# Optimization experiments

Measured on AMD Instinct MI355X. Metric: run time of the kernel, lower is better.

Reference implementation:

```python
import jax, jax.numpy as jnp
import numpy as np

B, N, C_IN, F, OUT = 32, 1000, 128, 128, 64
RATIOS = (0.8, 0.8)


def setup_inputs() -> dict:
    key = jax.random.key(0)
    ks = jax.random.split(key, 10)
    N_nodes = jax.random.randint(ks[0], (B,), 500, N + 1, dtype=jnp.int32)
    ar = jnp.arange(N)
    mask = (ar[None, :] < N_nodes[:, None]).astype(jnp.float32)  # [B,N]
    A = (jax.random.uniform(ks[1], (B, N, N)) < 0.02).astype(jnp.float32)
    A = A * (1.0 - jnp.eye(N, dtype=jnp.float32))
    A = jnp.maximum(A, A.transpose(0, 2, 1))  # symmetric, no self loops
    A = A * mask[:, :, None] * mask[:, None, :]
    x = jax.random.normal(ks[2], (B, N, C_IN)) * mask[..., None]

    def lin(k, fin, fout):
        bnd = 1.0 / np.sqrt(fin)
        kw, kb = jax.random.split(k)
        W = jax.random.uniform(kw, (fout, fin), minval=-bnd, maxval=bnd)
        b = jax.random.uniform(kb, (fout,), minval=-bnd, maxval=bnd)
        return W, b

    W0, b0 = lin(ks[3], C_IN, F)
    W1, b1 = lin(ks[4], F, F)
    W2, b2 = lin(ks[5], F, F)
    bnd = 1.0 / np.sqrt(F)
    p0 = jax.random.uniform(ks[6], (F, 1), minval=-bnd, maxval=bnd)
    p1 = jax.random.uniform(ks[7], (F, 1), minval=-bnd, maxval=bnd)
    Wfc, bfc = lin(ks[8], F, OUT)
    return dict(x=x, A=A, mask=mask, N_nodes=N_nodes,
                W0=W0, b0=b0, W1=W1, b1=b1, W2=W2, b2=b2,
                p0=p0, p1=p1, Wfc=Wfc, bfc=bfc)


def _gconv(x, A, mask, W, b):
    # K=1 Kipf-Welling conv: L = D^-1/2 (A+I) D^-1/2; relu(Linear(L x)) * mask
    n = A.shape[1]
    A_hat = A + jnp.eye(n, dtype=A.dtype)
    D = (jnp.sum(A_hat, axis=1) + 1e-5) ** -0.5  # [B,N]
    L = D[:, :, None] * A_hat * D[:, None, :]
    h = jnp.einsum('bij,bjc->bic', L, x)
    h = h @ W.T + b
    return jax.nn.relu(h) * mask[..., None]


def _pool(x, A, mask, N_nodes, p, ratio):
    # score each node, drop the N_remove lowest-scoring valid nodes per graph
    y = (x @ p)[..., 0] / jnp.sqrt(jnp.sum(p ** 2))  # [B,N]
    N_remove = (N_nodes.astype(jnp.float32) * (1.0 - ratio)).astype(jnp.int32)
    y_key = jnp.where(mask > 0, y, jnp.inf)  # invalid nodes rank last
    ranks = jnp.argsort(jnp.argsort(y_key, axis=1), axis=1)  # ascending rank
    new_mask = ((ranks >= N_remove[:, None]) & (mask > 0)).astype(x.dtype)
    x = x * jnp.tanh(y)[..., None] * new_mask[..., None]
    A = new_mask[:, :, None] * A * new_mask[:, None, :]
    return x, A, new_mask, N_nodes - N_remove


def reference(x, A, mask, N_nodes, W0, b0, W1, b1, W2, b2, p0, p1, Wfc, bfc):
    h = _gconv(x, A, mask, W0, b0)
    h, A1, m1, n1 = _pool(h, A, mask, N_nodes, p0, RATIOS[0])
    h = _gconv(h, A1, m1, W1, b1)
    h, A2, m2, n2 = _pool(h, A1, m1, n1, p1, RATIOS[1])
    h = _gconv(h, A2, m2, W2, b2)
    g = jnp.max(h, axis=1)  # [B,F] global max pool
    return g @ Wfc.T + bfc  # [B,OUT]
```

## Files before the change

### kernel.cpp

```cpp
#include <hip/hip_runtime.h>
#include <math.h>

#define BB 32
#define NN 1000
#define CC 128
#define FF 128
#define OO 64
#define CAP 128
#define NB 40

#define RMC ((float)(1.0 - 0.8))

__global__ void k_csr(const float* __restrict__ A, const float* __restrict__ mask,
                      const int* __restrict__ Nn,
                      const float* __restrict__ p0, const float* __restrict__ p1,
                      const float* __restrict__ W0, const float* __restrict__ W1,
                      const float* __restrict__ W2,
                      short* __restrict__ idx, int* __restrict__ cnt,
                      float* __restrict__ D, float* __restrict__ dg,
                      float* __restrict__ m, float* __restrict__ gate,
                      int* __restrict__ ncur0, float* __restrict__ pn,
                      float* __restrict__ Wt){
  int i = blockIdx.x, b = blockIdx.y, lane = threadIdx.x;
  if (i == NN){
    for (int j = lane; j < NN; j += 64){
      float v = mask[b*NN + j]; m[b*NN + j] = v; gate[b*NN + j] = v;
    }
    if (lane == 0) ncur0[b] = Nn[b];
    if (b == 0 && lane == 1){ float s=0.f; for(int c=0;c<FF;c++) s += p0[c]*p0[c]; pn[0] = sqrtf(s); }
    if (b == 1 && lane == 1){ float s=0.f; for(int c=0;c<FF;c++) s += p1[c]*p1[c]; pn[1] = sqrtf(s); }
    for (int e = b*1536 + lane; e < (b+1)*1536; e += 64){
      int s = e / (FF*CC), rem = e % (FF*CC);
      int c = rem >> 7, f = rem & 127;
      const float* W = (s == 0) ? W0 : (s == 1) ? W1 : W2;
      Wt[(size_t)s*FF*CC + rem] = W[f*CC + c];
    }
    return;
  }
  if (mask[b*NN + i] == 0.f){
    if (lane == 0){
      cnt[b*NN + i] = 0;
      D[b*NN + i]  = 1.0f / sqrtf(1.0f + 1e-5f);
      dg[b*NN + i] = 0.f;
    }
    return;
  }
  const float4* row = (const float4*)(A + ((size_t)b*NN + i)*NN);
  short* out = idx + ((size_t)b*NN + i)*CAP;
  int count = 0;
  for (int base = 0; base < 250; base += 64){
    int q = base + lane;
    float4 v;
    if (q < 250) v = row[q]; else { v.x=v.y=v.z=v.w=0.f; }
    int lc = (v.x!=0.f) + (v.y!=0.f) + (v.z!=0.f) + (v.w!=0.f);
    int pre = lc;
    #pragma unroll
    for (int off = 1; off < 64; off <<= 1){
      int t = __shfl_up(pre, off);
      if (lane >= off) pre += t;
    }
    int tot = __shfl(pre, 63);
    pre -= lc;
    int slot = count + pre;
    int j = q*4;
    if (v.x!=0.f && slot < CAP) out[slot++] = (short)j;
    if (v.y!=0.f && slot < CAP) out[slot++] = (short)(j+1);
    if (v.z!=0.f && slot < CAP) out[slot++] = (short)(j+2);
    if (v.w!=0.f && slot < CAP) out[slot++] = (short)(j+3);
    count += tot;
  }
  if (lane == 0){
    int cn = (count < CAP) ? count : CAP;
    cnt[b*NN + i] = cn;
    float Dv = 1.0f / sqrtf((float)cn + 1.0f + 1e-5f);
    D[b*NN + i]  = Dv;
    dg[b*NN + i] = Dv;
  }
}

__global__ void k_aggt(const short* __restrict__ idx, const int* __restrict__ cnt,
                       const float* __restrict__ D, const float* __restrict__ dg,
                       const float* __restrict__ m, const float* __restrict__ gate,
                       const float* __restrict__ h, float* __restrict__ T){
  __shared__ int   nb[4][CAP];
  __shared__ float dn[4][CAP];
  int blk = blockIdx.x;
  int b   = (blk & 7) + 8*((blk >> 3) & 3);
  int rem = blk >> 5;
  int tid = threadIdx.x;
  int w = tid >> 6, lane = tid & 63;
  int i = rem*4 + w;
  int g = lane >> 5, l32 = lane & 31;
  size_t orow = ((size_t)b*NN + i)*CC;
  const float* hb = h + (size_t)b*NN*CC;
  if (m[b*NN + i] == 0.f){
    if (g == 0){ float4 z = {0.f,0.f,0.f,0.f}; *(float4*)(T + orow + (l32<<2)) = z; }
    return;
  }
  int n = cnt[b*NN + i];
  const short* r = idx + ((size_t)b*NN + i)*CAP;
  int*   nbw = nb[w];
  float* dnw = dn[w];
  int j0 = 0; float d0 = 0.f; bool k0 = false;
  if (lane < n){ j0 = (int)r[lane]; d0 = dg[b*NN + j0]; k0 = (d0 != 0.f); }
  unsigned long long bal = __ballot(k0);
  int pre = __popcll(bal & ((1ull << lane) - 1ull));
  if (k0){ nbw[pre] = j0*CC; dnw[pre] = d0; }
  int nlive = __popcll(bal);
  if (n > 64){
    int e = lane + 64; int j1 = 0; float d1 = 0.f; bool k1 = false;
    if (e < n){ j1 = (int)r[e]; d1 = dg[b*NN + j1]; k1 = (d1 != 0.f); }
    unsigned long long bal1 = __ballot(k1);
    int pre1 = __popcll(bal1 & ((1ull << lane) - 1ull));
    if (k1){ nbw[nlive + pre1] = j1*CC; dnw[nlive + pre1] = d1; }
    nlive += __popcll(bal1);
  }
  int np = (nlive + 7) & ~7;
  if (lane < np - nlive){ nbw[nlive + lane] = 0; dnw[nlive + lane] = 0.f; }
  __builtin_amdgcn_wave_barrier();
  float4 a0 = {0.f,0.f,0.f,0.f}, a1 = a0, a2 = a0, a3 = a0;
  for (int k = 0; k < np; k += 8){
    int e = k + g;
    float4 v0 = *(const float4*)(hb + nbw[e  ] + (l32<<2));
    float4 v1 = *(const float4*)(hb + nbw[e+2] + (l32<<2));
    float4 v2 = *(const float4*)(hb + nbw[e+4] + (l32<<2));
    float4 v3 = *(const float4*)(hb + nbw[e+6] + (l32<<2));
    float e0 = dnw[e], e1 = dnw[e+2], e2 = dnw[e+4], e3 = dnw[e+6];
    a0.x += e0*v0.x; a0.y += e0*v0.y; a0.z += e0*v0.z; a0.w += e0*v0.w;
    a1.x += e1*v1.x; a1.y += e1*v1.y; a1.z += e1*v1.z; a1.w += e1*v1.w;
    a2.x += e2*v2.x; a2.y += e2*v2.y; a2.z += e2*v2.z; a2.w += e2*v2.w;
    a3.x += e3*v3.x; a3.y += e3*v3.y; a3.z += e3*v3.z; a3.w += e3*v3.w;
  }
  float4 Y;
  Y.x = (a0.x + a1.x) + (a2.x + a3.x);
  Y.y = (a0.y + a1.y) + (a2.y + a3.y);
  Y.z = (a0.z + a1.z) + (a2.z + a3.z);
  Y.w = (a0.w + a1.w) + (a2.w + a3.w);
  Y.x += __shfl_xor(Y.x, 32);
  Y.y += __shfl_xor(Y.y, 32);
  Y.z += __shfl_xor(Y.z, 32);
  Y.w += __shfl_xor(Y.w, 32);
  float Di = D[b*NN + i];
  float gi = gate[b*NN + i];
  if (g == 0){
    float4 hv = *(const float4*)(hb + (size_t)i*CC + (l32<<2));
    float4 o;
    o.x = Di*Y.x + Di*Di*(gi*hv.x);
    o.y = Di*Y.y + Di*Di*(gi*hv.y);
    o.z = Di*Y.z + Di*Di*(gi*hv.z);
    o.w = Di*Y.w + Di*Di*(gi*hv.w);
    *(float4*)(T + orow + (l32<<2)) = o;
  }
}

__global__ void k_lin(const float* __restrict__ T, const float* __restrict__ m,
                      const float* __restrict__ Wt,
                      const float* __restrict__ bias, float* __restrict__ Hout){
  __shared__ float t[NB][CC];
  int b = blockIdx.y, tid = threadIdx.x;
  int i0 = blockIdx.x * NB;
  const float4* Tg = (const float4*)(T + ((size_t)b*NN + i0)*CC);
  float4* tl = (float4*)&t[0][0];
  #pragma unroll
  for (int e = 0; e < 5; e++) tl[tid + e*256] = Tg[tid + e*256];
  __syncthreads();
  int fg = tid & 31;
  int nr = tid >> 5;
  float acc[5][4];
  float4 bi = ((const float4*)bias)[fg];
  #pragma unroll
  for (int n5 = 0; n5 < 5; n5++){
    acc[n5][0]=bi.x; acc[n5][1]=bi.y; acc[n5][2]=bi.z; acc[n5][3]=bi.w;
  }
  for (int c4 = 0; c4 < 32; c4++){
    float4 tv[5];
    #pragma unroll
    for (int n5 = 0; n5 < 5; n5++)
      tv[n5] = *((const float4*)&t[nr + n5*8][c4*4]);
    #pragma unroll
    for (int k = 0; k < 4; k++){
      float4 wv = ((const float4*)Wt)[(size_t)(c4*4 + k)*32 + fg];
      #pragma unroll
      for (int n5 = 0; n5 < 5; n5++){
        float tvv = (k==0) ? tv[n5].x : (k==1) ? tv[n5].y : (k==2) ? tv[n5].z : tv[n5].w;
        acc[n5][0] += tvv*wv.x; acc[n5][1] += tvv*wv.y;
        acc[n5][2] += tvv*wv.z; acc[n5][3] += tvv*wv.w;
      }
    }
  }
  #pragma unroll
  for (int n5 = 0; n5 < 5; n5++){
    int i = i0 + nr + n5*8;
    float mi = m[b*NN + i];
    float4 o4;
    o4.x = fmaxf(acc[n5][0], 0.f)*mi;
    o4.y = fmaxf(acc[n5][1], 0.f)*mi;
    o4.z = fmaxf(acc[n5][2], 0.f)*mi;
    o4.w = fmaxf(acc[n5][3], 0.f)*mi;
    ((float4*)&Hout[((size_t)b*NN + i)*CC])[fg] = o4;
  }
}

__global__ void k_score(const float* __restrict__ H, const float* __restrict__ p,
                        const float* __restrict__ pn, float* __restrict__ y){
  int i = blockIdx.x, b = blockIdx.y, lane = threadIdx.x;
  const float* hrow = H + ((size_t)b*NN + i)*CC;
  float s = hrow[lane]*p[lane] + hrow[lane+64]*p[lane+64];
  for (int off = 32; off > 0; off >>= 1) s += __shfl_down(s, off);
  if (lane == 0) y[b*NN + i] = s / pn[0];
}

__global__ void k_pool(const float* __restrict__ y, float* __restrict__ m,
                       const int* __restrict__ ncur_in, int* __restrict__ ncur_out,
                       float* __restrict__ gate){
  __shared__ float yk[NN];
  int b = blockIdx.y, tid = threadIdx.x;
  int i = blockIdx.x*256 + tid;
  for (int j = tid; j < NN; j += 256)
    yk[j] = (m[b*NN + j] > 0.f) ? y[b*NN + j] : INFINITY;
  __syncthreads();
  int n = ncur_in[b];
  int nr = (int)((float)n * RMC);
  float myv = (i < NN) ? yk[i] : INFINITY;
  int cnt = 0;
  const float4* yk4 = (const float4*)yk;
  #pragma unroll 5
  for (int q = 0; q < 250; q++){
    float4 v = yk4[q];
    int j0 = q*4;
    cnt += (int)((v.x < myv) || (v.x == myv && j0     < i));
    cnt += (int)((v.y < myv) || (v.y == myv && j0 + 1 < i));
    cnt += (int)((v.z < myv) || (v.z == myv && j0 + 2 < i));
    cnt += (int)((v.w < myv) || (v.w == myv && j0 + 3 < i));
  }
  if (i < NN){
    bool keep = (cnt >= nr) && (m[b*NN + i] > 0.f);
    m[b*NN + i]    = keep ? 1.0f : 0.0f;
    gate[b*NN + i] = keep ? tanhf(y[b*NN + i]) : 0.0f;
  }
  if (blockIdx.x == 0 && tid == 0) ncur_out[b] = n - nr;
}

__global__ void k_deg(const short* __restrict__ idx, const int* __restrict__ cnt,
                      const float* __restrict__ m, const float* __restrict__ gate,
                      float* __restrict__ D, float* __restrict__ dg){
  __shared__ float ml[NN];
  int b = blockIdx.y, tid = threadIdx.x;
  for (int i = tid; i < NN; i += 256) ml[i] = m[b*NN + i];
  __syncthreads();
  int j = blockIdx.x*250 + tid;
  if (tid < 250){
    const short* r = idx + ((size_t)b*NN + j)*CAP;
    int n = cnt[b*NN + j];
    float s0=0.f, s1=0.f, s2=0.f, s3=0.f;
    int k = 0;
    for (; k+4 <= n; k += 4){
      s0 += ml[r[k]]; s1 += ml[r[k+1]]; s2 += ml[r[k+2]]; s3 += ml[r[k+3]];
    }
    for (; k < n; k++) s0 += ml[r[k]];
    float Dv = 1.0f / sqrtf(((s0+s1)+(s2+s3)) + 1.0f + 1e-5f);
    D[b*NN + j]  = Dv;
    dg[b*NN + j] = Dv * gate[b*NN + j];
  }
}

__global__ void k_fmax(const float* __restrict__ H, const float* __restrict__ m,
                       float* __restrict__ part){
  int sx = blockIdx.x, b = blockIdx.y, c = threadIdx.x;
  float mx = 0.f;
  int i0 = sx*125;
  for (int i = i0; i < i0+125; i++){
    if (m[b*NN + i] != 0.f)
      mx = fmaxf(mx, H[((size_t)b*NN + i)*CC + c]);
  }
  part[((size_t)b*8 + sx)*CC + c] = mx;
}

__global__ void k_fc(const float* __restrict__ part, const float* __restrict__ Wfc,
                     const float* __restrict__ bfc, float* __restrict__ out){
  __shared__ float g[FF];
  int b = blockIdx.x, tid = threadIdx.x;
  float mx = 0.f;
  #pragma unroll
  for (int s = 0; s < 8; s++) mx = fmaxf(mx, part[((size_t)b*8 + s)*CC + tid]);
  g[tid] = mx;
  __syncthreads();
  if (tid < OO){
    float acc = bfc[tid];
    for (int c = 0; c < FF; c++) acc += g[c]*Wfc[tid*FF + c];
    out[b*OO + tid] = acc;
  }
}

extern "C" void kernel_launch(void* const* d_in, const int* in_sizes, int n_in,
                              void* d_out, int out_size, void* d_ws, size_t ws_size,
                              hipStream_t stream) {
  const float* x    = (const float*)d_in[0];
  const float* A    = (const float*)d_in[1];
  const float* mask = (const float*)d_in[2];
  const int*   Nn   = (const int*)  d_in[3];
  const float* W0   = (const float*)d_in[4];
  const float* b0   = (const float*)d_in[5];
  const float* W1   = (const float*)d_in[6];
  const float* b1   = (const float*)d_in[7];
  const float* W2   = (const float*)d_in[8];
  const float* b2   = (const float*)d_in[9];
  const float* p0   = (const float*)d_in[10];
  const float* p1   = (const float*)d_in[11];
  const float* Wfc  = (const float*)d_in[12];
  const float* bfc  = (const float*)d_in[13];
  float* out = (float*)d_out;

  char* w = (char*)d_ws;
  float* H   = (float*)w; w += (size_t)BB*NN*CC*4;
  float* T   = (float*)w; w += (size_t)BB*NN*CC*4;
  short* idx = (short*)w; w += (size_t)BB*NN*CAP*2;
  float* Wt  = (float*)w; w += (size_t)3*FF*CC*4;
  float* part= (float*)w; w += (size_t)8*BB*CC*4;
  int*   cnt = (int*)w;   w += (size_t)BB*NN*4;
  float* D   = (float*)w; w += (size_t)BB*NN*4;
  float* m   = (float*)w; w += (size_t)BB*NN*4;
  float* ysc = (float*)w; w += (size_t)BB*NN*4;
  float* gate= (float*)w; w += (size_t)BB*NN*4;
  float* dg  = (float*)w; w += (size_t)BB*NN*4;
  int*   ncur= (int*)w;   w += 3*BB*sizeof(int);
  float* pn  = (float*)w; w += 64;

  k_csr<<<dim3(NN + 1, BB), 64, 0, stream>>>(A, mask, Nn, p0, p1, W0, W1, W2,
                                             idx, cnt, D, dg, m, gate, ncur, pn, Wt);

  k_aggt<<<(BB*NN)/4, 256, 0, stream>>>(idx, cnt, D, dg, m, gate, x, T);
  k_lin<<<dim3(25, BB), 256, 0, stream>>>(T, m, Wt + 0*FF*CC, b0, H);
  k_score<<<dim3(NN, BB), 64, 0, stream>>>(H, p0, pn + 0, ysc);
  k_pool<<<dim3(4, BB), 256, 0, stream>>>(ysc, m, ncur + 0*BB, ncur + 1*BB, gate);
  k_deg<<<dim3(4, BB), 256, 0, stream>>>(idx, cnt, m, gate, D, dg);

  k_aggt<<<(BB*NN)/4, 256, 0, stream>>>(idx, cnt, D, dg, m, gate, H, T);
  k_lin<<<dim3(25, BB), 256, 0, stream>>>(T, m, Wt + 1*FF*CC, b1, H);
  k_score<<<dim3(NN, BB), 64, 0, stream>>>(H, p1, pn + 1, ysc);
  k_pool<<<dim3(4, BB), 256, 0, stream>>>(ysc, m, ncur + 1*BB, ncur + 2*BB, gate);
  k_deg<<<dim3(4, BB), 256, 0, stream>>>(idx, cnt, m, gate, D, dg);

  k_aggt<<<(BB*NN)/4, 256, 0, stream>>>(idx, cnt, D, dg, m, gate, H, T);
  k_lin<<<dim3(25, BB), 256, 0, stream>>>(T, m, Wt + 2*FF*CC, b2, H);

  k_fmax<<<dim3(8, BB), 128, 0, stream>>>(H, m, part);
  k_fc<<<BB, 128, 0, stream>>>(part, Wfc, bfc, out);
}
```

Baseline: 465.2 us.

## Fuse score, pool and degree kernels; merge max-pool with final FC

Replaces the separate score, rank-pool and degree kernels with a single per-graph kernel of 1024 threads that computes scores into shared memory, ranks nodes, updates mask and gate, and recomputes degree normalisation. The global max pool and final linear layer are also combined into one kernel. This removes several launches and the global-memory round trips through the intermediate score, mask and partial-max buffers. The cost is that each stage now runs on only 32 blocks (one per graph), which leaves much of the GPU idle and serialises the score computation within a block.

```diff
diff --git a/kernel.cpp b/kernel.cpp
--- a/kernel.cpp
+++ b/kernel.cpp
@@ -201,93 +201,100 @@
   }
 }
 
-__global__ void k_score(const float* __restrict__ H, const float* __restrict__ p,
-                        const float* __restrict__ pn, float* __restrict__ y){
-  int i = blockIdx.x, b = blockIdx.y, lane = threadIdx.x;
-  const float* hrow = H + ((size_t)b*NN + i)*CC;
-  float s = hrow[lane]*p[lane] + hrow[lane+64]*p[lane+64];
-  for (int off = 32; off > 0; off >>= 1) s += __shfl_down(s, off);
-  if (lane == 0) y[b*NN + i] = s / pn[0];
-}
-
-__global__ void k_pool(const float* __restrict__ y, float* __restrict__ m,
-                       const int* __restrict__ ncur_in, int* __restrict__ ncur_out,
-                       float* __restrict__ gate){
+__global__ void k_spd(const float* __restrict__ H, const float* __restrict__ p,
+                      const float* __restrict__ pn,
+                      const short* __restrict__ idx, const int* __restrict__ cnt,
+                      float* __restrict__ m, float* __restrict__ gate,
+                      const int* __restrict__ ncur_in, int* __restrict__ ncur_out,
+                      float* __restrict__ D, float* __restrict__ dg){
   __shared__ float yk[NN];
-  int b = blockIdx.y, tid = threadIdx.x;
-  int i = blockIdx.x*256 + tid;
-  for (int j = tid; j < NN; j += 256)
-    yk[j] = (m[b*NN + j] > 0.f) ? y[b*NN + j] : INFINITY;
+  __shared__ float ml[NN];
+  int b = blockIdx.x, tid = threadIdx.x;
+  int w = tid >> 6, lane = tid & 63;
+  float pl0 = p[lane], pl1 = p[lane + 64];
+  float pnv = pn[0];
+  for (int r = 0; r < 63; r++){
+    int i = w + (r << 4);
+    if (i < NN){
+      const float* hrow = H + ((size_t)b*NN + i)*CC;
+      float s = hrow[lane]*pl0 + hrow[lane+64]*pl1;
+      for (int off = 32; off > 0; off >>= 1) s += __shfl_down(s, off);
+      if (lane == 0) yk[i] = s / pnv;
+    }
+  }
+  __syncthreads();
+  float mold = 0.f;
+  if (tid < NN){
+    mold = m[b*NN + tid];
+    float v = yk[tid];
+    yk[tid] = (mold > 0.f) ? v : INFINITY;
+  }
   __syncthreads();
   int n = ncur_in[b];
   int nr = (int)((float)n * RMC);
+  int i = tid;
   float myv = (i < NN) ? yk[i] : INFINITY;
-  int cnt = 0;
+  int cn = 0;
   const float4* yk4 = (const float4*)yk;
   #pragma unroll 5
   for (int q = 0; q < 250; q++){
     float4 v = yk4[q];
     int j0 = q*4;
-    cnt += (int)((v.x < myv) || (v.x == myv && j0     < i));
-    cnt += (int)((v.y < myv) || (v.y == myv && j0 + 1 < i));
-    cnt += (int)((v.z < myv) || (v.z == myv && j0 + 2 < i));
-    cnt += (int)((v.w < myv) || (v.w == myv && j0 + 3 < i));
-  }
+    cn += (int)((v.x < myv) || (v.x == myv && j0     < i));
+    cn += (int)((v.y < myv) || (v.y == myv && j0 + 1 < i));
+    cn += (int)((v.z < myv) || (v.z == myv && j0 + 2 < i));
+    cn += (int)((v.w < myv) || (v.w == myv && j0 + 3 < i));
+  }
+  float gv = 0.f;
   if (i < NN){
-    bool keep = (cnt >= nr) && (m[b*NN + i] > 0.f);
+    bool keep = (cn >= nr) && (mold > 0.f);
+    gv = keep ? tanhf(yk[i]) : 0.f;
     m[b*NN + i]    = keep ? 1.0f : 0.0f;
-    gate[b*NN + i] = keep ? tanhf(y[b*NN + i]) : 0.0f;
-  }
-  if (blockIdx.x == 0 && tid == 0) ncur_out[b] = n - nr;
-}
-
-__global__ void k_deg(const short* __restrict__ idx, const int* __restrict__ cnt,
-                      const float* __restrict__ m, const float* __restrict__ gate,
-                      float* __restrict__ D, float* __restrict__ dg){
-  __shared__ float ml[NN];
-  int b = blockIdx.y, tid = threadIdx.x;
-  for (int i = tid; i < NN; i += 256) ml[i] = m[b*NN + i];
-  __syncthreads();
-  int j = blockIdx.x*250 + tid;
-  if (tid < 250){
-    const short* r = idx + ((size_t)b*NN + j)*CAP;
-    int n = cnt[b*NN + j];
+    gate[b*NN + i] = gv;
+    ml[i]          = keep ? 1.0f : 0.0f;
+  }
+  if (tid == 0) ncur_out[b] = n - nr;
+  __syncthreads();
+  if (tid < NN){
+    const short* r = idx + ((size_t)b*NN + tid)*CAP;
+    int ne = cnt[b*NN + tid];
     float s0=0.f, s1=0.f, s2=0.f, s3=0.f;
     int k = 0;
-    for (; k+4 <= n; k += 4){
+    for (; k+4 <= ne; k += 4){
       s0 += ml[r[k]]; s1 += ml[r[k+1]]; s2 += ml[r[k+2]]; s3 += ml[r[k+3]];
     }
-    for (; k < n; k++) s0 += ml[r[k]];
+    for (; k < ne; k++) s0 += ml[r[k]];
     float Dv = 1.0f / sqrtf(((s0+s1)+(s2+s3)) + 1.0f + 1e-5f);
-    D[b*NN + j]  = Dv;
-    dg[b*NN + j] = Dv * gate[b*NN + j];
-  }
-}
-
-__global__ void k_fmax(const float* __restrict__ H, const float* __restrict__ m,
-                       float* __restrict__ part){
-  int sx = blockIdx.x, b = blockIdx.y, c = threadIdx.x;
+    D[b*NN + tid]  = Dv;
+    dg[b*NN + tid] = Dv * gv;
+  }
+}
+
+__global__ void k_mfc(const float* __restrict__ H, const float* __restrict__ m,
+                      const float* __restrict__ Wfc, const float* __restrict__ bfc,
+                      float* __restrict__ out){
+  __shared__ float part[8][CC];
+  __shared__ float g[FF];
+  int b = blockIdx.x, tid = threadIdx.x;
+  int sx = tid >> 7, c = tid & 127;
   float mx = 0.f;
   int i0 = sx*125;
   for (int i = i0; i < i0+125; i++){
     if (m[b*NN + i] != 0.f)
       mx = fmaxf(mx, H[((size_t)b*NN + i)*CC + c]);
   }
-  part[((size_t)b*8 + sx)*CC + c] = mx;
-}
-
-__global__ void k_fc(const float* __restrict__ part, const float* __restrict__ Wfc,
-                     const float* __restrict__ bfc, float* __restrict__ out){
-  __shared__ float g[FF];
-  int b = blockIdx.x, tid = threadIdx.x;
-  float mx = 0.f;
-  #pragma unroll
-  for (int s = 0; s < 8; s++) mx = fmaxf(mx, part[((size_t)b*8 + s)*CC + tid]);
-  g[tid] = mx;
+  part[sx][c] = mx;
+  __syncthreads();
+  if (tid < FF){
+    float v = 0.f;
+    #pragma unroll
+    for (int s = 0; s < 8; s++) v = fmaxf(v, part[s][tid]);
+    g[tid] = v;
+  }
   __syncthreads();
   if (tid < OO){
     float acc = bfc[tid];
-    for (int c = 0; c < FF; c++) acc += g[c]*Wfc[tid*FF + c];
+    for (int c2 = 0; c2 < FF; c2++) acc += g[c2]*Wfc[tid*FF + c2];
     out[b*OO + tid] = acc;
   }
 }
@@ -325,25 +332,23 @@
   float* dg  = (float*)w; w += (size_t)BB*NN*4;
   int*   ncur= (int*)w;   w += 3*BB*sizeof(int);
   float* pn  = (float*)w; w += 64;
+  (void)part; (void)ysc;
 
   k_csr<<<dim3(NN + 1, BB), 64, 0, stream>>>(A, mask, Nn, p0, p1, W0, W1, W2,
                                              idx, cnt, D, dg, m, gate, ncur, pn, Wt);
 
   k_aggt<<<(BB*NN)/4, 256, 0, stream>>>(idx, cnt, D, dg, m, gate, x, T);
   k_lin<<<dim3(25, BB), 256, 0, stream>>>(T, m, Wt + 0*FF*CC, b0, H);
-  k_score<<<dim3(NN, BB), 64, 0, stream>>>(H, p0, pn + 0, ysc);
-  k_pool<<<dim3(4, BB), 256, 0, stream>>>(ysc, m, ncur + 0*BB, ncur + 1*BB, gate);
-  k_deg<<<dim3(4, BB), 256, 0, stream>>>(idx, cnt, m, gate, D, dg);
+  k_spd<<<BB, 1024, 0, stream>>>(H, p0, pn + 0, idx, cnt, m, gate,
+                                 ncur + 0*BB, ncur + 1*BB, D, dg);
 
   k_aggt<<<(BB*NN)/4, 256, 0, stream>>>(idx, cnt, D, dg, m, gate, H, T);
   k_lin<<<dim3(25, BB), 256, 0, stream>>>(T, m, Wt + 1*FF*CC, b1, H);
-  k_score<<<dim3(NN, BB), 64, 0, stream>>>(H, p1, pn + 1, ysc);
-  k_pool<<<dim3(4, BB), 256, 0, stream>>>(ysc, m, ncur + 1*BB, ncur + 2*BB, gate);
-  k_deg<<<dim3(4, BB), 256, 0, stream>>>(idx, cnt, m, gate, D, dg);
+  k_spd<<<BB, 1024, 0, stream>>>(H, p1, pn + 1, idx, cnt, m, gate,
+                                 ncur + 1*BB, ncur + 2*BB, D, dg);
 
   k_aggt<<<(BB*NN)/4, 256, 0, stream>>>(idx, cnt, D, dg, m, gate, H, T);
   k_lin<<<dim3(25, BB), 256, 0, stream>>>(T, m, Wt + 2*FF*CC, b2, H);
 
-  k_fmax<<<dim3(8, BB), 128, 0, stream>>>(H, m, part);
-  k_fc<<<BB, 128, 0, stream>>>(part, Wfc, bfc, out);
-}
+  k_mfc<<<BB, 1024, 0, stream>>>(H, m, Wfc, bfc, out);
+}
```

After: 567.6 us. 22.0% more time.

## Swizzle block-to-batch mapping across XCDs, copy input x, unroll gather loop

Applied to the files above, without the earlier changes.

Every kernel's 2D grid becomes a 1D grid whose block index is decoded so that consecutive blocks (round-robined across the 8 XCDs) map to graph b = r8 + 8*k. Each XCD then works on a fixed subset of graphs, which is meant to keep per-graph data local in that XCD's L2. A new k_xpin kernel copies x into a workspace buffer with the same swizzle, and the first aggregation reads that copy. The neighbour gather loop in k_aggt is unrolled from 8 to 16 entries per iteration with padding to 16, raising memory-level parallelism at the cost of more padded work and registers. The extra copy kernel adds a full pass over x.

```diff
diff --git a/kernel.cpp b/kernel.cpp
--- a/kernel.cpp
+++ b/kernel.cpp
@@ -10,6 +10,17 @@
 #define NB 40
 
 #define RMC ((float)(1.0 - 0.8))
+
+
+__global__ void k_xpin(const float* __restrict__ x, float* __restrict__ xp){
+  int blk = blockIdx.x;
+  int r = blk & 7, t = blk >> 3;
+  int b = r + 8*(t/125), seg = t % 125;
+  size_t base = ((size_t)b*NN + seg*8)*CC;
+  const float4* src = (const float4*)(x + base);
+  float4* dst = (float4*)(xp + base);
+  dst[threadIdx.x] = src[threadIdx.x];
+}
 
 __global__ void k_csr(const float* __restrict__ A, const float* __restrict__ mask,
                       const int* __restrict__ Nn,
@@ -21,7 +32,9 @@
                       float* __restrict__ m, float* __restrict__ gate,
                       int* __restrict__ ncur0, float* __restrict__ pn,
                       float* __restrict__ Wt){
-  int i = blockIdx.x, b = blockIdx.y, lane = threadIdx.x;
+  int blk = blockIdx.x, lane = threadIdx.x;
+  int r8 = blk & 7, t = blk >> 3;
+  int b = r8 + 8*(t/1001), i = t % 1001;
   if (i == NN){
     for (int j = lane; j < NN; j += 64){
       float v = mask[b*NN + j]; m[b*NN + j] = v; gate[b*NN + j] = v;
@@ -56,8 +69,8 @@
     int pre = lc;
     #pragma unroll
     for (int off = 1; off < 64; off <<= 1){
-      int t = __shfl_up(pre, off);
-      if (lane >= off) pre += t;
+      int t2 = __shfl_up(pre, off);
+      if (lane >= off) pre += t2;
     }
     int tot = __shfl(pre, 63);
     pre -= lc;
@@ -115,21 +128,30 @@
     if (k1){ nbw[nlive + pre1] = j1*CC; dnw[nlive + pre1] = d1; }
     nlive += __popcll(bal1);
   }
-  int np = (nlive + 7) & ~7;
+  int np = (nlive + 15) & ~15;
   if (lane < np - nlive){ nbw[nlive + lane] = 0; dnw[nlive + lane] = 0.f; }
   __builtin_amdgcn_wave_barrier();
   float4 a0 = {0.f,0.f,0.f,0.f}, a1 = a0, a2 = a0, a3 = a0;
-  for (int k = 0; k < np; k += 8){
+  for (int k = 0; k < np; k += 16){
     int e = k + g;
-    float4 v0 = *(const float4*)(hb + nbw[e  ] + (l32<<2));
-    float4 v1 = *(const float4*)(hb + nbw[e+2] + (l32<<2));
-    float4 v2 = *(const float4*)(hb + nbw[e+4] + (l32<<2));
-    float4 v3 = *(const float4*)(hb + nbw[e+6] + (l32<<2));
+    float4 v0 = *(const float4*)(hb + nbw[e   ] + (l32<<2));
+    float4 v1 = *(const float4*)(hb + nbw[e+ 2] + (l32<<2));
+    float4 v2 = *(const float4*)(hb + nbw[e+ 4] + (l32<<2));
+    float4 v3 = *(const float4*)(hb + nbw[e+ 6] + (l32<<2));
+    float4 v4 = *(const float4*)(hb + nbw[e+ 8] + (l32<<2));
+    float4 v5 = *(const float4*)(hb + nbw[e+10] + (l32<<2));
+    float4 v6 = *(const float4*)(hb + nbw[e+12] + (l32<<2));
+    float4 v7 = *(const float4*)(hb + nbw[e+14] + (l32<<2));
     float e0 = dnw[e], e1 = dnw[e+2], e2 = dnw[e+4], e3 = dnw[e+6];
+    float e4 = dnw[e+8], e5 = dnw[e+10], e6 = dnw[e+12], e7 = dnw[e+14];
     a0.x += e0*v0.x; a0.y += e0*v0.y; a0.z += e0*v0.z; a0.w += e0*v0.w;
     a1.x += e1*v1.x; a1.y += e1*v1.y; a1.z += e1*v1.z; a1.w += e1*v1.w;
     a2.x += e2*v2.x; a2.y += e2*v2.y; a2.z += e2*v2.z; a2.w += e2*v2.w;
     a3.x += e3*v3.x; a3.y += e3*v3.y; a3.z += e3*v3.z; a3.w += e3*v3.w;
+    a0.x += e4*v4.x; a0.y += e4*v4.y; a0.z += e4*v4.z; a0.w += e4*v4.w;
+    a1.x += e5*v5.x; a1.y += e5*v5.y; a1.z += e5*v5.z; a1.w += e5*v5.w;
+    a2.x += e6*v6.x; a2.y += e6*v6.y; a2.z += e6*v6.z; a2.w += e6*v6.w;
+    a3.x += e7*v7.x; a3.y += e7*v7.y; a3.z += e7*v7.z; a3.w += e7*v7.w;
   }
   float4 Y;
   Y.x = (a0.x + a1.x) + (a2.x + a3.x);
@@ -157,8 +179,10 @@
                       const float* __restrict__ Wt,
                       const float* __restrict__ bias, float* __restrict__ Hout){
   __shared__ float t[NB][CC];
-  int b = blockIdx.y, tid = threadIdx.x;
-  int i0 = blockIdx.x * NB;
+  int blk = blockIdx.x, tid = threadIdx.x;
+  int r8 = blk & 7, tq = blk >> 3;
+  int b = r8 + 8*(tq/25);
+  int i0 = (tq % 25) * NB;
   const float4* Tg = (const float4*)(T + ((size_t)b*NN + i0)*CC);
   float4* tl = (float4*)&t[0][0];
   #pragma unroll
@@ -203,7 +227,9 @@
 
 __global__ void k_score(const float* __restrict__ H, const float* __restrict__ p,
                         const float* __restrict__ pn, float* __restrict__ y){
-  int i = blockIdx.x, b = blockIdx.y, lane = threadIdx.x;
+  int blk = blockIdx.x, lane = threadIdx.x;
+  int r8 = blk & 7, t = blk >> 3;
+  int b = r8 + 8*(t/1000), i = t % 1000;
   const float* hrow = H + ((size_t)b*NN + i)*CC;
   float s = hrow[lane]*p[lane] + hrow[lane+64]*p[lane+64];
   for (int off = 32; off > 0; off >>= 1) s += __shfl_down(s, off);
@@ -214,8 +240,10 @@
                        const int* __restrict__ ncur_in, int* __restrict__ ncur_out,
                        float* __restrict__ gate){
   __shared__ float yk[NN];
-  int b = blockIdx.y, tid = threadIdx.x;
-  int i = blockIdx.x*256 + tid;
+  int blk = blockIdx.x, tid = threadIdx.x;
+  int r8 = blk & 7, t = blk >> 3;
+  int b = r8 + 8*(t >> 2), xx = t & 3;
+  int i = xx*256 + tid;
   for (int j = tid; j < NN; j += 256)
     yk[j] = (m[b*NN + j] > 0.f) ? y[b*NN + j] : INFINITY;
   __syncthreads();
@@ -238,17 +266,19 @@
     m[b*NN + i]    = keep ? 1.0f : 0.0f;
     gate[b*NN + i] = keep ? tanhf(y[b*NN + i]) : 0.0f;
   }
-  if (blockIdx.x == 0 && tid == 0) ncur_out[b] = n - nr;
+  if (xx == 0 && tid == 0) ncur_out[b] = n - nr;
 }
 
 __global__ void k_deg(const short* __restrict__ idx, const int* __restrict__ cnt,
                       const float* __restrict__ m, const float* __restrict__ gate,
                       float* __restrict__ D, float* __restrict__ dg){
   __shared__ float ml[NN];
-  int b = blockIdx.y, tid = threadIdx.x;
+  int blk = blockIdx.x, tid = threadIdx.x;
+  int r8 = blk & 7, t = blk >> 3;
+  int b = r8 + 8*(t >> 2), xx = t & 3;
   for (int i = tid; i < NN; i += 256) ml[i] = m[b*NN + i];
   __syncthreads();
-  int j = blockIdx.x*250 + tid;
+  int j = xx*250 + tid;
   if (tid < 250){
     const short* r = idx + ((size_t)b*NN + j)*CAP;
     int n = cnt[b*NN + j];
@@ -266,7 +296,9 @@
 
 __global__ void k_fmax(const float* __restrict__ H, const float* __restrict__ m,
                        float* __restrict__ part){
-  int sx = blockIdx.x, b = blockIdx.y, c = threadIdx.x;
+  int blk = blockIdx.x, c = threadIdx.x;
+  int r8 = blk & 7, t = blk >> 3;
+  int b = r8 + 8*(t >> 3), sx = t & 7;
   float mx = 0.f;
   int i0 = sx*125;
   for (int i = i0; i < i0+125; i++){
@@ -325,25 +357,27 @@
   float* dg  = (float*)w; w += (size_t)BB*NN*4;
   int*   ncur= (int*)w;   w += 3*BB*sizeof(int);
   float* pn  = (float*)w; w += 64;
-
-  k_csr<<<dim3(NN + 1, BB), 64, 0, stream>>>(A, mask, Nn, p0, p1, W0, W1, W2,
-                                             idx, cnt, D, dg, m, gate, ncur, pn, Wt);
-
-  k_aggt<<<(BB*NN)/4, 256, 0, stream>>>(idx, cnt, D, dg, m, gate, x, T);
-  k_lin<<<dim3(25, BB), 256, 0, stream>>>(T, m, Wt + 0*FF*CC, b0, H);
-  k_score<<<dim3(NN, BB), 64, 0, stream>>>(H, p0, pn + 0, ysc);
-  k_pool<<<dim3(4, BB), 256, 0, stream>>>(ysc, m, ncur + 0*BB, ncur + 1*BB, gate);
-  k_deg<<<dim3(4, BB), 256, 0, stream>>>(idx, cnt, m, gate, D, dg);
+  float* xp  = (float*)w; w += (size_t)BB*NN*CC*4;
+
+  k_xpin<<<4000, 256, 0, stream>>>(x, xp);
+  k_csr<<<32032, 64, 0, stream>>>(A, mask, Nn, p0, p1, W0, W1, W2,
+                                  idx, cnt, D, dg, m, gate, ncur, pn, Wt);
+
+  k_aggt<<<(BB*NN)/4, 256, 0, stream>>>(idx, cnt, D, dg, m, gate, xp, T);
+  k_lin<<<800, 256, 0, stream>>>(T, m, Wt + 0*FF*CC, b0, H);
+  k_score<<<32000, 64, 0, stream>>>(H, p0, pn + 0, ysc);
+  k_pool<<<128, 256, 0, stream>>>(ysc, m, ncur + 0*BB, ncur + 1*BB, gate);
+  k_deg<<<128, 256, 0, stream>>>(idx, cnt, m, gate, D, dg);
 
   k_aggt<<<(BB*NN)/4, 256, 0, stream>>>(idx, cnt, D, dg, m, gate, H, T);
-  k_lin<<<dim3(25, BB), 256, 0, stream>>>(T, m, Wt + 1*FF*CC, b1, H);
-  k_score<<<dim3(NN, BB), 64, 0, stream>>>(H, p1, pn + 1, ysc);
-  k_pool<<<dim3(4, BB), 256, 0, stream>>>(ysc, m, ncur + 1*BB, ncur + 2*BB, gate);
-  k_deg<<<dim3(4, BB), 256, 0, stream>>>(idx, cnt, m, gate, D, dg);
+  k_lin<<<800, 256, 0, stream>>>(T, m, Wt + 1*FF*CC, b1, H);
+  k_score<<<32000, 64, 0, stream>>>(H, p1, pn + 1, ysc);
+  k_pool<<<128, 256, 0, stream>>>(ysc, m, ncur + 1*BB, ncur + 2*BB, gate);
+  k_deg<<<128, 256, 0, stream>>>(idx, cnt, m, gate, D, dg);
 
   k_aggt<<<(BB*NN)/4, 256, 0, stream>>>(idx, cnt, D, dg, m, gate, H, T);
-  k_lin<<<dim3(25, BB), 256, 0, stream>>>(T, m, Wt + 2*FF*CC, b2, H);
-
-  k_fmax<<<dim3(8, BB), 128, 0, stream>>>(H, m, part);
+  k_lin<<<800, 256, 0, stream>>>(T, m, Wt + 2*FF*CC, b2, H);
+
+  k_fmax<<<256, 128, 0, stream>>>(H, m, part);
   k_fc<<<BB, 128, 0, stream>>>(part, Wfc, bfc, out);
 }
```

Measured after the change: 449.9 us. 3.3% less time.
